# Kernel tuning notes

Hardware: AMD Instinct MI355X
Metric: run time of the kernel (lower is better)

The kernel has to match this reference:

```python
import jax, jax.numpy as jnp
import numpy as np

N_HEAD = 16
HEAD_DIM = 64  # n_embd // n_head = 1024 // 16

def setup_inputs() -> dict:
    key = jax.random.key(0)
    k1, k2, k3 = jax.random.split(key, 3)
    B, T, C = 4, 2048, 1024
    x = jax.random.normal(k1, (B, T, C), dtype=jnp.float32)
    w_qkv = jax.random.normal(k2, (3 * C, C), dtype=jnp.float32) * (C ** -0.5)
    w_proj = jax.random.normal(k3, (C, C), dtype=jnp.float32) * (C ** -0.5)
    b_proj = jnp.zeros((C,), dtype=jnp.float32)
    return {"x": x, "w_qkv": w_qkv, "w_proj": w_proj, "b_proj": b_proj}

def reference(x, w_qkv, w_proj, b_proj):
    B, T, C = x.shape
    H, hd = N_HEAD, HEAD_DIM
    # fused QKV projection (no bias), torch Linear: x @ W^T
    qkv = jnp.einsum('btc,dc->btd', x, w_qkv)           # [B,T,3C]
    # module-specific reshape: per-head groups of 3*hd, then chunk into q,k,v
    qkv = qkv.reshape(B, T, H, 3 * hd)
    q, k, v = jnp.split(qkv, 3, axis=-1)                # each [B,T,H,hd]
    q = q.transpose(0, 2, 1, 3)                         # [B,H,T,hd]
    k = k.transpose(0, 2, 1, 3)
    v = v.transpose(0, 2, 1, 3)
    att = jnp.einsum('bhqd,bhkd->bhqk', q, k) * (hd ** -0.5)
    causal = jnp.tril(jnp.ones((T, T), dtype=bool))
    att = jnp.where(causal, att, -jnp.inf)
    att = jax.nn.softmax(att, axis=-1)
    out = jnp.einsum('bhqk,bhkd->bhqd', att, v)         # [B,H,T,hd]
    out = out.transpose(0, 2, 1, 3).reshape(B, T, C)
    out = jnp.einsum('btc,dc->btd', out, w_proj) + b_proj
    return out
```

## Files before the change

### kernel.cpp

```cpp
#include <hip/hip_runtime.h>
#include <hip/hip_bf16.h>

typedef __attribute__((ext_vector_type(8))) short bf16x8;
typedef __attribute__((ext_vector_type(4))) float f32x4;
typedef __attribute__((ext_vector_type(16))) float f32x16;
typedef __attribute__((ext_vector_type(4))) int i32x4;
typedef unsigned short u16;

__device__ __forceinline__ u16 f2bf(float f) {
    __hip_bfloat16 h = __float2bfloat16(f);
    return __builtin_bit_cast(u16, h);
}
__device__ __forceinline__ bf16x8 load8(const u16* p) {
    return *reinterpret_cast<const bf16x8*>(p);
}
__device__ __forceinline__ void gl2lds16(const u16* g, u16* l) {
    __builtin_amdgcn_global_load_lds(
        (const __attribute__((address_space(1))) void*)g,
        (__attribute__((address_space(3))) void*)l, 16, 0, 0);
}
__device__ __forceinline__ unsigned int cvtpk(float lo, float hi) {
    unsigned int r;
    asm("v_cvt_pk_bf16_f32 %0, %1, %2" : "=v"(r) : "v"(lo), "v"(hi));
    return r;
}

#define QSCALE 0.1803368801111244f

__global__ __launch_bounds__(256) void cast_f32_bf16(
    const float* __restrict__ src, u16* __restrict__ dst, int n4)
{
    int i = blockIdx.x * blockDim.x + threadIdx.x;
    if (i < n4) {
        float4 f = reinterpret_cast<const float4*>(src)[i];
        ushort4 o;
        o.x = f2bf(f.x); o.y = f2bf(f.y); o.z = f2bf(f.z); o.w = f2bf(f.w);
        reinterpret_cast<ushort4*>(dst)[i] = o;
    }
}

#define GEMM128_BODY(EPILOGUE)                                                 \
    const int t = threadIdx.x;                                                 \
    const int lane = t & 63;                                                   \
    const int wave = t >> 6;                                                   \
    const int quad = lane >> 4;                                                \
    const int lid  = lane & 15;                                                \
    const int wrow = wave & 1;                                                 \
    const int wcol = wave >> 1;                                                \
    const int mtile = blockIdx.x * 128;                                        \
    const int ntile = blockIdx.y * 128;                                        \
    const int srow = t >> 2;                                                   \
    const int scol = (t & 3) * 8;                                              \
    const u16* ga0 = Aptr + (size_t)(mtile + srow) * 1024 + scol;              \
    const u16* ga1 = Aptr + (size_t)(mtile + 64 + srow) * 1024 + scol;         \
    const u16* gb0 = Bptr + (size_t)(ntile + srow) * 1024 + scol;              \
    const u16* gb1 = Bptr + (size_t)(ntile + 64 + srow) * 1024 + scol;         \
    u16* la0 = As + t * 8;                                                     \
    u16* la1 = As + (256 + t) * 8;                                             \
    u16* lb0 = Bs + t * 8;                                                     \
    u16* lb1 = Bs + (256 + t) * 8;                                             \
    f32x4 acc[4][4] = {};                                                      \
    const int aro = wrow * 64 * 32 + quad * 8;                                 \
    const int bro = wcol * 64 * 32 + quad * 8;                                 \
    for (int k0 = 0; k0 < 1024; k0 += 32) {                                    \
        __syncthreads();                                                       \
        gl2lds16(ga0 + k0, la0);                                               \
        gl2lds16(ga1 + k0, la1);                                               \
        gl2lds16(gb0 + k0, lb0);                                               \
        gl2lds16(gb1 + k0, lb1);                                               \
        __syncthreads();                                                       \
        bf16x8 a[4], b[4];                                                     \
        _Pragma("unroll")                                                      \
        for (int i = 0; i < 4; ++i) {                                          \
            a[i] = load8(As + aro + (i * 16 + lid) * 32);                      \
            b[i] = load8(Bs + bro + (i * 16 + lid) * 32);                      \
        }                                                                      \
        _Pragma("unroll")                                                      \
        for (int mi = 0; mi < 4; ++mi)                                         \
            _Pragma("unroll")                                                  \
            for (int ni = 0; ni < 4; ++ni)                                     \
                acc[mi][ni] = __builtin_amdgcn_mfma_f32_16x16x32_bf16(         \
                    a[mi], b[ni], acc[mi][ni], 0, 0, 0);                       \
    }                                                                          \
    EPILOGUE

__global__ __launch_bounds__(256) void qkv_gemm128(
    const u16* __restrict__ Aptr, const u16* __restrict__ Bptr,
    u16* __restrict__ Q, u16* __restrict__ K, u16* __restrict__ Vt)
{
    __shared__ __align__(16) u16 smem[8320];
    u16* const As = smem;
    u16* const Bs = smem + 4096;
    GEMM128_BODY(
    __syncthreads();
    _Pragma("unroll")
    for (int mi = 0; mi < 4; ++mi)
        _Pragma("unroll")
        for (int ni = 0; ni < 4; ++ni)
            _Pragma("unroll")
            for (int r = 0; r < 4; ++r) {
                int ml = wrow * 64 + mi * 16 + quad * 4 + r;
                int m = mtile + ml;
                int n = ntile + wcol * 64 + ni * 16 + lid;
                int h = n / 192;
                int rr = n - h * 192;
                int sel = rr >> 6;
                int d = rr & 63;
                float v = acc[mi][ni][r];
                if (sel == 2)
                    smem[d * 130 + ml] = f2bf(v);
                else if (sel == 0)
                    Q[((size_t)h * 8192 + m) * 64 + d] = f2bf(v * QSCALE);
                else
                    K[((size_t)h * 8192 + m) * 64 + d] = f2bf(v);
            }
    __syncthreads();
    for (int d = wave; d < 64; d += 4) {
        int lo = ntile - 128 - d;
        int hh = (lo + 191) / 192;
        int n2 = hh * 192 + 128 + d;
        if (n2 >= ntile && n2 < ntile + 128 && hh < 16) {
            unsigned int w = (unsigned int)smem[d * 130 + lane * 2]
                           | ((unsigned int)smem[d * 130 + lane * 2 + 1] << 16);
            *reinterpret_cast<unsigned int*>(
                Vt + ((size_t)(hh * 64 + d)) * 8192 + mtile + lane * 2) = w;
        }
    }
    )
}

__global__ __launch_bounds__(256) void proj_gemm128(
    const u16* __restrict__ Aptr, const u16* __restrict__ Bptr,
    const float* __restrict__ bias, float* __restrict__ out)
{
    __shared__ __align__(16) u16 smem[8192];
    u16* const As = smem;
    u16* const Bs = smem + 4096;
    GEMM128_BODY(
    _Pragma("unroll")
    for (int mi = 0; mi < 4; ++mi)
        _Pragma("unroll")
        for (int ni = 0; ni < 4; ++ni)
            _Pragma("unroll")
            for (int r = 0; r < 4; ++r) {
                int m = mtile + wrow * 64 + mi * 16 + quad * 4 + r;
                int n = ntile + wcol * 64 + ni * 16 + lid;
                out[(size_t)m * 1024 + n] = acc[mi][ni][r] + bias[n];
            }
    )
}

__global__ __launch_bounds__(128, 4) void attn(
    const u16* __restrict__ Q, const u16* __restrict__ K,
    const u16* __restrict__ Vtg, u16* __restrict__ O)
{
    const int qt64 = 31 - (blockIdx.x >> 6);
    const int bh = blockIdx.x & 63;
    const int b = bh >> 4, h = bh & 15;
    const int tid = threadIdx.x;
    const int lane = tid & 63;
    const int wave = tid >> 6;
    const int c31 = lane & 31;
    const int ht  = lane >> 5;

    const size_t hb = ((size_t)h * 8192 + (size_t)b * 2048) * 64;
    const u16* Qp = Q + hb;
    const u16* Kp = K + hb;
    const u16* Vp = Vtg + (size_t)h * 64 * 8192 + (size_t)b * 2048;

    __shared__ __align__(16) u16 Vt[2][64 * 64];

    const int vd = tid >> 3, vslot = tid & 7;
    const int vchunk = vslot ^ (vd & 7);
    const u16* vg = Vp + (size_t)vd * 8192 + vchunk * 8;
    u16* const ldst = (u16*)Vt[0] + vd * 64 + vslot * 8;

#define STAGE(BUFSEL, KK)                                                      \
    {                                                                          \
        u16* d_ = ldst + (BUFSEL) * 4096;                                      \
        _Pragma("unroll")                                                      \
        for (int g = 0; g < 4; ++g)                                            \
            gl2lds16(vg + (size_t)g * 16 * 8192 + (KK), d_ + g * 1024);        \
    }

    const int qw = qt64 * 64 + wave * 32;
    const int q  = qw + c31;

    bf16x8 qf[4];
#pragma unroll
    for (int dm = 0; dm < 4; ++dm)
        qf[dm] = load8(Qp + (size_t)q * 64 + dm * 16 + ht * 8);

    f32x16 od0 = {}, od1 = {};
    float lsum = 0.f;

    const int nkt = qt64 + 1;

    STAGE(0, 0)

#define SOFTMAX_KB(ST, KBOFF, PF0, PF1)                                        \
    {                                                                          \
        float pv[16];                                                          \
        _Pragma("unroll")                                                      \
        for (int r = 0; r < 16; ++r) {                                         \
            const int kg = k0 + (KBOFF) + (r & 3) + 8 * (r >> 2) + 4 * ht;     \
            float sv = ST[r];                                                  \
            if (needmask && kg > q) sv = -1e30f;                               \
            const float p = exp2f(sv);                                         \
            pv[r] = p;                                                         \
            lsum += p;                                                         \
        }                                                                      \
        _Pragma("unroll")                                                      \
        for (int a = 0; a < 2; ++a) {                                          \
            unsigned int u  = cvtpk(pv[8 * a + 0], pv[8 * a + 1]);             \
            unsigned int u2 = cvtpk(pv[8 * a + 2], pv[8 * a + 3]);             \
            unsigned int v  = cvtpk(pv[8 * a + 4], pv[8 * a + 5]);             \
            unsigned int v2 = cvtpk(pv[8 * a + 6], pv[8 * a + 7]);             \
            int r1 = __shfl_xor((int)(ht ? u : v), 32, 64);                    \
            int r2 = __shfl_xor((int)(ht ? u2 : v2), 32, 64);                  \
            i32x4 w;                                                           \
            w.x = ht ? r1 : (int)u;                                            \
            w.y = ht ? r2 : (int)u2;                                           \
            w.z = ht ? (int)v : r1;                                            \
            w.w = ht ? (int)v2 : r2;                                           \
            ((a) ? (PF1) : (PF0)) = __builtin_bit_cast(bf16x8, w);             \
        }                                                                      \
    }

    for (int kt = 0; kt < nkt; ++kt) {
        const int k0 = kt * 64;
        u16* vbuf = Vt[kt & 1];
        const bool skipB = (k0 >= qw);
        const bool needmask = (k0 + 63 > qw);
        bf16x8 pf[4];

        {
            bf16x8 kfA[4];
#pragma unroll
            for (int dm = 0; dm < 4; ++dm)
                kfA[dm] = load8(Kp + (size_t)(k0 + c31) * 64 + dm * 16 + ht * 8);
            f32x16 stA = {};
            __builtin_amdgcn_s_setprio(1);
#pragma unroll
            for (int dm = 0; dm < 4; ++dm)
                stA = __builtin_amdgcn_mfma_f32_32x32x16_bf16(kfA[dm], qf[dm], stA, 0, 0, 0);
            __builtin_amdgcn_s_setprio(0);
            SOFTMAX_KB(stA, 0, pf[0], pf[1]);
        }
        if (!skipB) {
            bf16x8 kfB[4];
#pragma unroll
            for (int dm = 0; dm < 4; ++dm)
                kfB[dm] = load8(Kp + (size_t)(k0 + 32 + c31) * 64 + dm * 16 + ht * 8);
            f32x16 stB = {};
            __builtin_amdgcn_s_setprio(1);
#pragma unroll
            for (int dm = 0; dm < 4; ++dm)
                stB = __builtin_amdgcn_mfma_f32_32x32x16_bf16(kfB[dm], qf[dm], stB, 0, 0, 0);
            __builtin_amdgcn_s_setprio(0);
            SOFTMAX_KB(stB, 32, pf[2], pf[3]);
        }

        __syncthreads();

        if (kt + 1 < nkt) STAGE((kt + 1) & 1, k0 + 64)

        __builtin_amdgcn_s_setprio(1);
#pragma unroll
        for (int km = 0; km < 4; ++km) {
            if (km >= 2 && skipB) continue;
            const int sl = ((km * 2 + ht) ^ (c31 & 7)) * 8;
            bf16x8 v0 = load8(vbuf + c31 * 64 + sl);
            bf16x8 v1 = load8(vbuf + (32 + c31) * 64 + sl);
            od0 = __builtin_amdgcn_mfma_f32_32x32x16_bf16(v0, pf[km], od0, 0, 0, 0);
            od1 = __builtin_amdgcn_mfma_f32_32x32x16_bf16(v1, pf[km], od1, 0, 0, 0);
        }
        __builtin_amdgcn_s_setprio(0);
    }

    const float tot = lsum +
        __builtin_bit_cast(float, __shfl_xor(__builtin_bit_cast(int, lsum), 32, 64));
    const float inv = 1.0f / tot;

    const size_t orow = (size_t)(b * 2048 + q) * 1024 + h * 64;
#pragma unroll
    for (int tp = 0; tp < 8; ++tp) {
        const int r = 2 * tp;
        const int d = (r & 3) + 8 * (r >> 2) + 4 * ht;
        unsigned int w0 = (unsigned int)f2bf(od0[r] * inv) |
                          ((unsigned int)f2bf(od0[r + 1] * inv) << 16);
        unsigned int w1 = (unsigned int)f2bf(od1[r] * inv) |
                          ((unsigned int)f2bf(od1[r + 1] * inv) << 16);
        *reinterpret_cast<unsigned int*>(const_cast<u16*>(O) + orow + d) = w0;
        *reinterpret_cast<unsigned int*>(const_cast<u16*>(O) + orow + 32 + d) = w1;
    }
#undef SOFTMAX_KB
#undef STAGE
}

extern "C" void kernel_launch(void* const* d_in, const int* in_sizes, int n_in,
                              void* d_out, int out_size, void* d_ws, size_t ws_size,
                              hipStream_t stream) {
    const float* x      = (const float*)d_in[0];
    const float* w_qkv  = (const float*)d_in[1];
    const float* w_proj = (const float*)d_in[2];
    const float* b_proj = (const float*)d_in[3];
    float* out = (float*)d_out;

    u16* Q   = (u16*)d_ws;
    u16* K   = Q   + (size_t)16 * 8192 * 64;
    u16* Vt  = K   + (size_t)16 * 8192 * 64;
    u16* A2  = Vt  + (size_t)16 * 64 * 8192;
    u16* Xb  = A2  + (size_t)8192 * 1024;
    u16* Wqb = Xb  + (size_t)8192 * 1024;
    u16* Wpb = Wqb + (size_t)3072 * 1024;

    cast_f32_bf16<<<dim3(8192), 256, 0, stream>>>(x, Xb, 8192 * 1024 / 4);
    cast_f32_bf16<<<dim3(3072), 256, 0, stream>>>(w_qkv, Wqb, 3072 * 1024 / 4);
    cast_f32_bf16<<<dim3(1024), 256, 0, stream>>>(w_proj, Wpb, 1024 * 1024 / 4);

    qkv_gemm128<<<dim3(64, 24), 256, 0, stream>>>(Xb, Wqb, Q, K, Vt);
    attn<<<dim3(2048), 128, 0, stream>>>(Q, K, Vt, A2);
    proj_gemm128<<<dim3(64, 8), 256, 0, stream>>>(A2, Wpb, b_proj, out);
}
```

Before: 289.9 us.

## Use 256x128 double-buffered GEMM tiles with BK=64 and fuse cast kernels

Replaces the 128x128 single-buffered GEMMs with 256x128 tiles run by 512 threads, a K step of 64, and double-buffered LDS so the next tile's global-to-LDS loads overlap the current MFMAs. MFMA priority is raised with s_setprio, and the three cast launches are merged into one kernel. This cuts barriers per K step and launch overhead and increases reuse per tile. The costs are 96KB of dynamic LDS per block and fewer blocks, which may reduce occupancy, and the proj GEMM now has only 256 blocks.

```diff
diff --git a/kernel.cpp b/kernel.cpp
--- a/kernel.cpp
+++ b/kernel.cpp
@@ -27,71 +27,92 @@
 
 #define QSCALE 0.1803368801111244f
 
-__global__ __launch_bounds__(256) void cast_f32_bf16(
-    const float* __restrict__ src, u16* __restrict__ dst, int n4)
+__global__ __launch_bounds__(256) void cast_all(
+    const float* __restrict__ x, const float* __restrict__ wq,
+    const float* __restrict__ wp, u16* __restrict__ Xb,
+    u16* __restrict__ Wqb, u16* __restrict__ Wpb)
 {
     int i = blockIdx.x * blockDim.x + threadIdx.x;
-    if (i < n4) {
-        float4 f = reinterpret_cast<const float4*>(src)[i];
-        ushort4 o;
-        o.x = f2bf(f.x); o.y = f2bf(f.y); o.z = f2bf(f.z); o.w = f2bf(f.w);
-        reinterpret_cast<ushort4*>(dst)[i] = o;
-    }
-}
-
-#define GEMM128_BODY(EPILOGUE)                                                 \
+    const float* s; u16* d; int j;
+    if (i < 2097152)      { s = x;  d = Xb;  j = i; }
+    else if (i < 2883584) { s = wq; d = Wqb; j = i - 2097152; }
+    else                  { s = wp; d = Wpb; j = i - 2883584; }
+    float4 f = reinterpret_cast<const float4*>(s)[j];
+    ushort4 o;
+    o.x = f2bf(f.x); o.y = f2bf(f.y); o.z = f2bf(f.z); o.w = f2bf(f.w);
+    reinterpret_cast<ushort4*>(d)[j] = o;
+}
+
+#define GEMM256_BODY(EPILOGUE)                                                 \
     const int t = threadIdx.x;                                                 \
     const int lane = t & 63;                                                   \
     const int wave = t >> 6;                                                   \
-    const int quad = lane >> 4;                                                \
+    const int quad = (lane >> 4);                                              \
     const int lid  = lane & 15;                                                \
-    const int wrow = wave & 1;                                                 \
-    const int wcol = wave >> 1;                                                \
-    const int mtile = blockIdx.x * 128;                                        \
+    const int wm = wave >> 1;                                                  \
+    const int wn = wave & 1;                                                   \
+    const int mtile = blockIdx.x * 256;                                        \
     const int ntile = blockIdx.y * 128;                                        \
     const int srow = t >> 2;                                                   \
-    const int scol = (t & 3) * 8;                                              \
-    const u16* ga0 = Aptr + (size_t)(mtile + srow) * 1024 + scol;              \
-    const u16* ga1 = Aptr + (size_t)(mtile + 64 + srow) * 1024 + scol;         \
-    const u16* gb0 = Bptr + (size_t)(ntile + srow) * 1024 + scol;              \
-    const u16* gb1 = Bptr + (size_t)(ntile + 64 + srow) * 1024 + scol;         \
-    u16* la0 = As + t * 8;                                                     \
-    u16* la1 = As + (256 + t) * 8;                                             \
-    u16* lb0 = Bs + t * 8;                                                     \
-    u16* lb1 = Bs + (256 + t) * 8;                                             \
+    const int sk   = (t & 3) * 8;                                              \
+    const u16* gA0 = Aptr + (size_t)(mtile + srow) * 1024 + sk;                \
+    const u16* gA1 = Aptr + (size_t)(mtile + 128 + srow) * 1024 + sk;          \
+    const u16* gA2 = gA0 + 32;                                                 \
+    const u16* gA3 = gA1 + 32;                                                 \
+    const u16* gB0 = Bptr + (size_t)(ntile + srow) * 1024 + sk;                \
+    const u16* gB1 = gB0 + 32;                                                 \
     f32x4 acc[4][4] = {};                                                      \
-    const int aro = wrow * 64 * 32 + quad * 8;                                 \
-    const int bro = wcol * 64 * 32 + quad * 8;                                 \
-    for (int k0 = 0; k0 < 1024; k0 += 32) {                                    \
+    STAGE_G(smem, 0)                                                           \
+    for (int ks = 0; ks < 16; ++ks) {                                          \
+        u16* cb = smem + (ks & 1) * 24576;                                     \
         __syncthreads();                                                       \
-        gl2lds16(ga0 + k0, la0);                                               \
-        gl2lds16(ga1 + k0, la1);                                               \
-        gl2lds16(gb0 + k0, lb0);                                               \
-        gl2lds16(gb1 + k0, lb1);                                               \
-        __syncthreads();                                                       \
-        bf16x8 a[4], b[4];                                                     \
-        _Pragma("unroll")                                                      \
-        for (int i = 0; i < 4; ++i) {                                          \
-            a[i] = load8(As + aro + (i * 16 + lid) * 32);                      \
-            b[i] = load8(Bs + bro + (i * 16 + lid) * 32);                      \
+        if (ks + 1 < 16) {                                                     \
+            u16* nb = smem + ((ks + 1) & 1) * 24576;                           \
+            STAGE_G(nb, (ks + 1) * 64)                                         \
         }                                                                      \
+        bf16x8 af[4][2], bfr[4][2];                                            \
         _Pragma("unroll")                                                      \
         for (int mi = 0; mi < 4; ++mi)                                         \
             _Pragma("unroll")                                                  \
-            for (int ni = 0; ni < 4; ++ni)                                     \
+            for (int kh = 0; kh < 2; ++kh)                                     \
+                af[mi][kh] = load8(cb + kh * 8192 +                            \
+                    (wm * 64 + mi * 16 + lid) * 32 + quad * 8);                \
+        _Pragma("unroll")                                                      \
+        for (int ni = 0; ni < 4; ++ni)                                         \
+            _Pragma("unroll")                                                  \
+            for (int kh = 0; kh < 2; ++kh)                                     \
+                bfr[ni][kh] = load8(cb + 16384 + kh * 4096 +                   \
+                    (wn * 64 + ni * 16 + lid) * 32 + quad * 8);                \
+        __builtin_amdgcn_s_setprio(1);                                         \
+        _Pragma("unroll")                                                      \
+        for (int mi = 0; mi < 4; ++mi)                                         \
+            _Pragma("unroll")                                                  \
+            for (int ni = 0; ni < 4; ++ni) {                                   \
                 acc[mi][ni] = __builtin_amdgcn_mfma_f32_16x16x32_bf16(         \
-                    a[mi], b[ni], acc[mi][ni], 0, 0, 0);                       \
+                    af[mi][0], bfr[ni][0], acc[mi][ni], 0, 0, 0);              \
+                acc[mi][ni] = __builtin_amdgcn_mfma_f32_16x16x32_bf16(         \
+                    af[mi][1], bfr[ni][1], acc[mi][ni], 0, 0, 0);              \
+            }                                                                  \
+        __builtin_amdgcn_s_setprio(0);                                         \
     }                                                                          \
     EPILOGUE
 
-__global__ __launch_bounds__(256) void qkv_gemm128(
+#define STAGE_G(BASE, KK)                                                      \
+    {                                                                          \
+        gl2lds16(gA0 + (KK), (BASE) + t * 8);                                  \
+        gl2lds16(gA1 + (KK), (BASE) + 4096 + t * 8);                           \
+        gl2lds16(gA2 + (KK), (BASE) + 8192 + t * 8);                           \
+        gl2lds16(gA3 + (KK), (BASE) + 12288 + t * 8);                          \
+        gl2lds16(gB0 + (KK), (BASE) + 16384 + t * 8);                          \
+        gl2lds16(gB1 + (KK), (BASE) + 20480 + t * 8);                          \
+    }
+
+__global__ __launch_bounds__(512, 2) void qkv_gemm256(
     const u16* __restrict__ Aptr, const u16* __restrict__ Bptr,
     u16* __restrict__ Q, u16* __restrict__ K, u16* __restrict__ Vt)
 {
-    __shared__ __align__(16) u16 smem[8320];
-    u16* const As = smem;
-    u16* const Bs = smem + 4096;
-    GEMM128_BODY(
+    extern __shared__ u16 smem[];
+    GEMM256_BODY(
     __syncthreads();
     _Pragma("unroll")
     for (int mi = 0; mi < 4; ++mi)
@@ -99,52 +120,54 @@
         for (int ni = 0; ni < 4; ++ni)
             _Pragma("unroll")
             for (int r = 0; r < 4; ++r) {
-                int ml = wrow * 64 + mi * 16 + quad * 4 + r;
+                int ml = wm * 64 + mi * 16 + quad * 4 + r;
                 int m = mtile + ml;
-                int n = ntile + wcol * 64 + ni * 16 + lid;
+                int n = ntile + wn * 64 + ni * 16 + lid;
                 int h = n / 192;
                 int rr = n - h * 192;
                 int sel = rr >> 6;
                 int d = rr & 63;
                 float v = acc[mi][ni][r];
                 if (sel == 2)
-                    smem[d * 130 + ml] = f2bf(v);
+                    smem[d * 258 + ml] = f2bf(v);
                 else if (sel == 0)
                     Q[((size_t)h * 8192 + m) * 64 + d] = f2bf(v * QSCALE);
                 else
                     K[((size_t)h * 8192 + m) * 64 + d] = f2bf(v);
             }
     __syncthreads();
-    for (int d = wave; d < 64; d += 4) {
+    for (int d = wave; d < 64; d += 8) {
         int lo = ntile - 128 - d;
         int hh = (lo + 191) / 192;
         int n2 = hh * 192 + 128 + d;
         if (n2 >= ntile && n2 < ntile + 128 && hh < 16) {
-            unsigned int w = (unsigned int)smem[d * 130 + lane * 2]
-                           | ((unsigned int)smem[d * 130 + lane * 2 + 1] << 16);
-            *reinterpret_cast<unsigned int*>(
-                Vt + ((size_t)(hh * 64 + d)) * 8192 + mtile + lane * 2) = w;
+            _Pragma("unroll")
+            for (int p = 0; p < 2; ++p) {
+                int idx = lane + p * 64;
+                unsigned int w = (unsigned int)smem[d * 258 + idx * 2]
+                               | ((unsigned int)smem[d * 258 + idx * 2 + 1] << 16);
+                *reinterpret_cast<unsigned int*>(
+                    Vt + ((size_t)(hh * 64 + d)) * 8192 + mtile + idx * 2) = w;
+            }
         }
     }
     )
 }
 
-__global__ __launch_bounds__(256) void proj_gemm128(
+__global__ __launch_bounds__(512, 2) void proj_gemm256(
     const u16* __restrict__ Aptr, const u16* __restrict__ Bptr,
     const float* __restrict__ bias, float* __restrict__ out)
 {
-    __shared__ __align__(16) u16 smem[8192];
-    u16* const As = smem;
-    u16* const Bs = smem + 4096;
-    GEMM128_BODY(
+    extern __shared__ u16 smem[];
+    GEMM256_BODY(
     _Pragma("unroll")
     for (int mi = 0; mi < 4; ++mi)
         _Pragma("unroll")
         for (int ni = 0; ni < 4; ++ni)
             _Pragma("unroll")
             for (int r = 0; r < 4; ++r) {
-                int m = mtile + wrow * 64 + mi * 16 + quad * 4 + r;
-                int n = ntile + wcol * 64 + ni * 16 + lid;
+                int m = mtile + wm * 64 + mi * 16 + quad * 4 + r;
+                int n = ntile + wn * 64 + ni * 16 + lid;
                 out[(size_t)m * 1024 + n] = acc[mi][ni][r] + bias[n];
             }
     )
@@ -315,11 +338,9 @@
     u16* Wqb = Xb  + (size_t)8192 * 1024;
     u16* Wpb = Wqb + (size_t)3072 * 1024;
 
-    cast_f32_bf16<<<dim3(8192), 256, 0, stream>>>(x, Xb, 8192 * 1024 / 4);
-    cast_f32_bf16<<<dim3(3072), 256, 0, stream>>>(w_qkv, Wqb, 3072 * 1024 / 4);
-    cast_f32_bf16<<<dim3(1024), 256, 0, stream>>>(w_proj, Wpb, 1024 * 1024 / 4);
-
-    qkv_gemm128<<<dim3(64, 24), 256, 0, stream>>>(Xb, Wqb, Q, K, Vt);
+    cast_all<<<dim3(12288), 256, 0, stream>>>(x, w_qkv, w_proj, Xb, Wqb, Wpb);
+
+    qkv_gemm256<<<dim3(32, 24), 512, 98304, stream>>>(Xb, Wqb, Q, K, Vt);
     attn<<<dim3(2048), 128, 0, stream>>>(Q, K, Vt, A2);
-    proj_gemm128<<<dim3(64, 8), 256, 0, stream>>>(A2, Wpb, b_proj, out);
-}
+    proj_gemm256<<<dim3(32, 8), 512, 98304, stream>>>(A2, Wpb, b_proj, out);
+}
```

New measurement: 278.3 us. -4.0%, faster.
